# Optimization experiments

Measured on AMD Instinct MI355X. Metric: run time of the kernel, lower is better.

## Reference

```python
import jax, jax.numpy as jnp
import numpy as np

N_FFT = 512
HOP = 128
WIN = 512
LENGTH = 600  # hardcoded in the original forward


def _hann(n):
    # torch.hann_window default is periodic: 0.5*(1-cos(2*pi*i/n))
    i = jnp.arange(n, dtype=jnp.float32)
    return 0.5 * (1.0 - jnp.cos(2.0 * jnp.pi * i / n))


def setup_inputs() -> dict:
    key = jax.random.key(0)
    x = jax.random.normal(key, (8192, 1, 257, 6, 2), dtype=jnp.float32)
    return {"x": x}


def reference(x):
    B, C, F, T, D = x.shape  # C==1, F==n_fft//2+1, D==2
    # view(B, F, T, D) + view_as_complex
    spec = x[:, 0, :, :, 0] + 1j * x[:, 0, :, :, 1]          # [B, F, T] complex64
    # inverse real FFT per frame (torch.istft, normalized=False, onesided=True)
    frames = jnp.fft.irfft(spec.transpose(0, 2, 1), n=N_FFT, axis=-1)  # [B, T, n_fft]
    win = _hann(WIN)                                          # [n_fft] (win_length == n_fft)
    frames = frames * win                                     # synthesis windowing
    # overlap-add
    L = HOP * (T - 1) + N_FFT
    idx = jnp.arange(T)[:, None] * HOP + jnp.arange(N_FFT)[None, :]  # [T, n_fft]
    y = jnp.zeros((B, L), dtype=frames.dtype).at[:, idx].add(frames)  # [B, L]
    # window-square envelope normalization (COLA division)
    env = jnp.zeros((L,), dtype=frames.dtype).at[idx].add(win * win)  # [L]
    # center=True trim of n_fft//2, then length=600 crop
    start = N_FFT // 2
    sig = y[:, start:start + LENGTH] / env[start:start + LENGTH]       # [B, 600]
    return sig[:, None, :]                                    # unsqueeze(1) -> [B, 1, 600]
```

## Files before the change

### kernel.cpp

```cpp
#include <hip/hip_runtime.h>
#include <hip/hip_bf16.h>


#define NFFT   512
#define HOP    128
#define KDIM   3084
#define KP     3136
#define NOUT   600
#define NP     640
#define BM     64
#define BN     128
#define BK     64
#define KSTEPS (KP / BK)
#define LDA    72

#define NFRAG_K 98
#define FRAG_SH 512
#define WTOT    ((size_t)(NP / 16) * NFRAG_K * FRAG_SH)
#define NKSPLIT 4
#define GRIDB   (128 * 5 * NKSPLIT)

typedef short s16x8 __attribute__((ext_vector_type(8)));
typedef float f32x4 __attribute__((ext_vector_type(4)));

static __device__ __forceinline__ unsigned short bf16_bits(float f) {
    __hip_bfloat16 b = __float2bfloat16(f);
    return *(unsigned short*)&b;
}

static __device__ __forceinline__ void lds_barrier() {
    asm volatile("s_waitcnt lgkmcnt(0)" ::: "memory");
    __builtin_amdgcn_s_barrier();
    asm volatile("" ::: "memory");
}

__global__ __launch_bounds__(256) void gen_W(unsigned short* __restrict__ Wt,
                                             float4* __restrict__ outZ,
                                             int nvec4) {
    __shared__ float costab[512];
    __shared__ __align__(16) unsigned short rowbuf[KP];
    const int l   = blockIdx.x;
    const int tid = threadIdx.x;
    const float w0 = 6.283185307179586f / 512.0f;

    for (int i = blockIdx.x * 256 + tid; i < nvec4; i += NP * 256)
        outZ[i] = make_float4(0.f, 0.f, 0.f, 0.f);

    *(int4*)(rowbuf + tid * 8) = make_int4(0, 0, 0, 0);
    if (tid < 136) *(int4*)(rowbuf + (256 + tid) * 8) = make_int4(0, 0, 0, 0);
    costab[tid]       = __cosf((float)tid * w0);
    costab[tid + 256] = __cosf((float)(tid + 256) * w0);
    __syncthreads();

    if (l < NOUT) {
        const int p = l + 256;
        float env = 0.0f;
#pragma unroll
        for (int tt = 0; tt < 6; ++tt) {
            int m = p - HOP * tt;
            if (m >= 0 && m < NFFT) {
                float w = 0.5f - 0.5f * costab[m];
                env += w * w;
            }
        }
        const float inv = 1.0f / (512.0f * env);
        for (int f = tid; f <= 256; f += 256) {
            float cf = (f == 0 || f == 256) ? 1.0f : 2.0f;
#pragma unroll
            for (int t = 0; t < 6; ++t) {
                int n = p - HOP * t;
                if (n >= 0 && n < NFFT) {
                    float w = 0.5f - 0.5f * costab[n];
                    float scale = cf * w * inv;
                    int a = (f * n) & 511;
                    float c = costab[a];
                    float s = costab[(a + 384) & 511];
                    rowbuf[f * 12 + t * 2 + 0] = bf16_bits(scale * c);
                    rowbuf[f * 12 + t * 2 + 1] = bf16_bits(-scale * s);
                }
            }
        }
    }
    __syncthreads();

    const int n16 = l >> 4, r = l & 15;
    for (int u = tid; u < 392; u += 256) {
        const int kc = u >> 2, q = u & 3;
        int4 val = *(const int4*)(rowbuf + kc * 32 + q * 8);
        *(int4*)(Wt + (((size_t)n16 * NFRAG_K + kc) * 64 + q * 16 + r) * 8) = val;
    }
}

__global__ __launch_bounds__(256, 4) void gemm_kernel(
        const float* __restrict__ X,
        const unsigned short* __restrict__ Wt,
        float* __restrict__ out) {
    __shared__ __align__(16) unsigned short As[2 * BM * LDA];

    const int tid = threadIdx.x;
    const int bid  = blockIdx.x;
    const int xcd  = bid & 7;
    const int rest = bid >> 3;
    const int mt   = xcd * 16 + rest / 20;
    const int sub  = rest % 20;
    const int nt   = sub >> 2;
    const int kidx = sub & 3;
    const int mBase = mt * BM;
    const int nBase = nt * BN;
    const int sBeg  = (kidx * KSTEPS) / NKSPLIT;
    const int sEnd  = ((kidx + 1) * KSTEPS) / NKSPLIT;

    const int lane = tid & 63;
    const int wave = tid >> 6;
    const int wm   = (wave & 1) * 32;
    const int wn   = (wave >> 1) * 64;
    const int lrow = lane & 15;
    const int quad = lane >> 4;

    const int aRow = tid >> 4, aU = tid & 15;
    const float* aPtr = X + (size_t)(mBase + aRow) * KDIM + sBeg * BK + aU * 4;
    const int aColBase = aU * 4;
    const size_t aRowStride = (size_t)16 * KDIM;

    const int n16base = nt * 8 + (wave >> 1) * 4;
    const unsigned short* wB0 = Wt + (size_t)n16base * NFRAG_K * FRAG_SH
                                   + (size_t)lane * 8;

    f32x4 acc[2][4];
#pragma unroll
    for (int i = 0; i < 2; ++i)
#pragma unroll
        for (int j = 0; j < 4; ++j) acc[i][j] = (f32x4){0.f, 0.f, 0.f, 0.f};

#define ISSUE_A(AV, s)                                                         \
    {                                                                          \
        const int k0_ = (s) * BK;                                              \
        _Pragma("unroll")                                                      \
        for (int p = 0; p < 4; ++p) {                                          \
            AV[p] = make_float4(0.f, 0.f, 0.f, 0.f);                           \
            if (k0_ + aColBase < KDIM)                                         \
                AV[p] = *(const float4*)(aPtr + (size_t)((s) - sBeg) * BK +    \
                                         p * aRowStride);                      \
        }                                                                      \
    }

#define ISSUE_B4(BV, s, ks)                                                    \
    {                                                                          \
        const size_t kc_ = (size_t)(2 * (s) + (ks));                           \
        _Pragma("unroll")                                                      \
        for (int j = 0; j < 4; ++j)                                            \
            BV[j] = *(const s16x8*)(const void*)(wB0 +                         \
                        ((size_t)j * NFRAG_K + kc_) * FRAG_SH);                \
    }

#define STAGE_A(AV, ABASE)                                                     \
    {                                                                          \
        _Pragma("unroll")                                                      \
        for (int p = 0; p < 4; ++p) {                                          \
            float4 v = AV[p];                                                  \
            unsigned long long pk = (unsigned long long)bf16_bits(v.x) |       \
                                    ((unsigned long long)bf16_bits(v.y) << 16) |\
                                    ((unsigned long long)bf16_bits(v.z) << 32) |\
                                    ((unsigned long long)bf16_bits(v.w) << 48); \
            *(unsigned long long*)(As + (ABASE) + (aRow + 16 * p) * LDA +      \
                                   aU * 4) = pk;                               \
        }                                                                      \
    }

#define COMPUTE_KS(ks, ABASE, BV)                                              \
    {                                                                          \
        const int koff = (ks) * 32 + quad * 8;                                 \
        s16x8 afr0 = *(const s16x8*)(const void*)(As + (ABASE) +               \
                         (wm + lrow) * LDA + koff);                            \
        s16x8 afr1 = *(const s16x8*)(const void*)(As + (ABASE) +               \
                         (wm + 16 + lrow) * LDA + koff);                       \
        _Pragma("unroll")                                                      \
        for (int j = 0; j < 4; ++j)                                            \
            acc[0][j] = __builtin_amdgcn_mfma_f32_16x16x32_bf16(               \
                afr0, BV[j], acc[0][j], 0, 0, 0);                              \
        _Pragma("unroll")                                                      \
        for (int j = 0; j < 4; ++j)                                            \
            acc[1][j] = __builtin_amdgcn_mfma_f32_16x16x32_bf16(               \
                afr1, BV[j], acc[1][j], 0, 0, 0);                              \
    }

    float4 avH[4];
    s16x8  bv0[4], bv1[4];
    ISSUE_A(avH, sBeg);
    ISSUE_B4(bv0, sBeg, 0);
    ISSUE_B4(bv1, sBeg, 1);
    STAGE_A(avH, 0);
    ISSUE_A(avH, sBeg + 1);
    lds_barrier();

    int ard = 0;
    for (int step = sBeg; step < sEnd; ++step) {
        const int awr = ard ^ (BM * LDA);
        if (step + 1 < sEnd) {
            STAGE_A(avH, awr);
            if (step + 2 < sEnd) ISSUE_A(avH, step + 2);
        }
        COMPUTE_KS(0, ard, bv0);
        if (step + 1 < sEnd) ISSUE_B4(bv0, step + 1, 0);
        COMPUTE_KS(1, ard, bv1);
        if (step + 1 < sEnd) ISSUE_B4(bv1, step + 1, 1);
        lds_barrier();
        ard = awr;
    }

#undef ISSUE_A
#undef ISSUE_B4
#undef STAGE_A
#undef COMPUTE_KS

#pragma unroll
    for (int i = 0; i < 2; ++i) {
#pragma unroll
        for (int j = 0; j < 4; ++j) {
            int gn = nBase + wn + j * 16 + lrow;
            if (gn < NOUT) {
#pragma unroll
                for (int r = 0; r < 4; ++r) {
                    int gm = mBase + wm + i * 16 + quad * 4 + r;
                    atomicAdd(out + (size_t)gm * NOUT + gn, acc[i][j][r]);
                }
            }
        }
    }
}

extern "C" void kernel_launch(void* const* d_in, const int* in_sizes, int n_in,
                              void* d_out, int out_size, void* d_ws, size_t ws_size,
                              hipStream_t stream) {
    const float* X = (const float*)d_in[0];
    unsigned short* W = (unsigned short*)d_ws;
    float* out = (float*)d_out;

    gen_W<<<dim3(NP), 256, 0, stream>>>(W, (float4*)d_out, out_size / 4);
    gemm_kernel<<<dim3(GRIDB), 256, 0, stream>>>(X, W, out);
}
```

Baseline: 265.0 us.

## Double M tile to 128 and peel the K tail into a direct-load epilogue

Raises the GEMM block tile from 64 to 128 rows, so each wave computes a 64x64 sub-tile and every loaded B fragment feeds twice as many MFMAs. This halves the grid and lowers the occupancy hint to 3. The K loop now runs 12 full steps per split with no bounds checks. The leftover 32-wide K fragment is handled by the last split, which reads A straight from global memory with per-element guards. The goal is better B reuse and fewer A-load branches, at the cost of more registers, fewer blocks and a scalar tail path.

Result: faster. 259.5 us (-2.1%).

```diff
diff --git a/kernel.cpp b/kernel.cpp
--- a/kernel.cpp
+++ b/kernel.cpp
@@ -8,17 +8,17 @@
 #define KP     3136
 #define NOUT   600
 #define NP     640
-#define BM     64
+#define BM     128
 #define BN     128
 #define BK     64
-#define KSTEPS (KP / BK)
 #define LDA    72
+#define ABUF   (BM * LDA)
 
 #define NFRAG_K 98
 #define FRAG_SH 512
 #define WTOT    ((size_t)(NP / 16) * NFRAG_K * FRAG_SH)
 #define NKSPLIT 4
-#define GRIDB   (128 * 5 * NKSPLIT)
+#define GRIDB   (64 * 5 * NKSPLIT)
 
 typedef short s16x8 __attribute__((ext_vector_type(8)));
 typedef float f32x4 __attribute__((ext_vector_type(4)));
@@ -91,121 +91,131 @@
     }
 }
 
-__global__ __launch_bounds__(256, 4) void gemm_kernel(
+__global__ __launch_bounds__(256, 3) void gemm_kernel(
         const float* __restrict__ X,
         const unsigned short* __restrict__ Wt,
         float* __restrict__ out) {
-    __shared__ __align__(16) unsigned short As[2 * BM * LDA];
+    __shared__ __align__(16) unsigned short As[2 * ABUF];
 
     const int tid = threadIdx.x;
     const int bid  = blockIdx.x;
     const int xcd  = bid & 7;
     const int rest = bid >> 3;
-    const int mt   = xcd * 16 + rest / 20;
+    const int mt   = xcd * 8 + rest / 20;
     const int sub  = rest % 20;
     const int nt   = sub >> 2;
     const int kidx = sub & 3;
     const int mBase = mt * BM;
     const int nBase = nt * BN;
-    const int sBeg  = (kidx * KSTEPS) / NKSPLIT;
-    const int sEnd  = ((kidx + 1) * KSTEPS) / NKSPLIT;
+    const int sBeg  = kidx * 12;
+    const int sEnd  = sBeg + 12;
 
     const int lane = tid & 63;
     const int wave = tid >> 6;
-    const int wm   = (wave & 1) * 32;
-    const int wn   = (wave >> 1) * 64;
+    const int wm2  = (wave & 1) * 64;
+    const int wn2  = (wave >> 1) * 64;
     const int lrow = lane & 15;
     const int quad = lane >> 4;
 
-    const int aRow = tid >> 4, aU = tid & 15;
-    const float* aPtr = X + (size_t)(mBase + aRow) * KDIM + sBeg * BK + aU * 4;
-    const int aColBase = aU * 4;
+    const int aRowS = tid >> 4, aU = tid & 15;
+    const float* aPtr = X + (size_t)(mBase + aRowS) * KDIM + sBeg * BK + aU * 4;
     const size_t aRowStride = (size_t)16 * KDIM;
 
     const int n16base = nt * 8 + (wave >> 1) * 4;
     const unsigned short* wB0 = Wt + (size_t)n16base * NFRAG_K * FRAG_SH
                                    + (size_t)lane * 8;
 
-    f32x4 acc[2][4];
-#pragma unroll
-    for (int i = 0; i < 2; ++i)
+    f32x4 acc[4][4];
+#pragma unroll
+    for (int i = 0; i < 4; ++i)
 #pragma unroll
         for (int j = 0; j < 4; ++j) acc[i][j] = (f32x4){0.f, 0.f, 0.f, 0.f};
 
-#define ISSUE_A(AV, s)                                                         \
-    {                                                                          \
-        const int k0_ = (s) * BK;                                              \
-        _Pragma("unroll")                                                      \
-        for (int p = 0; p < 4; ++p) {                                          \
-            AV[p] = make_float4(0.f, 0.f, 0.f, 0.f);                           \
-            if (k0_ + aColBase < KDIM)                                         \
-                AV[p] = *(const float4*)(aPtr + (size_t)((s) - sBeg) * BK +    \
-                                         p * aRowStride);                      \
-        }                                                                      \
-    }
-
-#define ISSUE_B4(BV, s, ks)                                                    \
-    {                                                                          \
-        const size_t kc_ = (size_t)(2 * (s) + (ks));                           \
+#define ISSUE_A(s)                                                             \
+    {                                                                          \
+        const float* b_ = aPtr + (size_t)((s) - sBeg) * BK;                    \
+        _Pragma("unroll")                                                      \
+        for (int p = 0; p < 8; ++p)                                            \
+            avH[p] = *(const float4*)(b_ + (size_t)p * aRowStride);            \
+    }
+
+#define ISSUE_B4(BV, kc_)                                                      \
+    {                                                                          \
         _Pragma("unroll")                                                      \
         for (int j = 0; j < 4; ++j)                                            \
             BV[j] = *(const s16x8*)(const void*)(wB0 +                         \
-                        ((size_t)j * NFRAG_K + kc_) * FRAG_SH);                \
-    }
-
-#define STAGE_A(AV, ABASE)                                                     \
-    {                                                                          \
-        _Pragma("unroll")                                                      \
-        for (int p = 0; p < 4; ++p) {                                          \
-            float4 v = AV[p];                                                  \
+                        ((size_t)j * NFRAG_K + (size_t)(kc_)) * FRAG_SH);      \
+    }
+
+#define STAGE_A(AB)                                                            \
+    {                                                                          \
+        _Pragma("unroll")                                                      \
+        for (int p = 0; p < 8; ++p) {                                          \
+            float4 v = avH[p];                                                 \
             unsigned long long pk = (unsigned long long)bf16_bits(v.x) |       \
                                     ((unsigned long long)bf16_bits(v.y) << 16) |\
                                     ((unsigned long long)bf16_bits(v.z) << 32) |\
                                     ((unsigned long long)bf16_bits(v.w) << 48); \
-            *(unsigned long long*)(As + (ABASE) + (aRow + 16 * p) * LDA +      \
+            *(unsigned long long*)(As + (AB) + (aRowS + 16 * p) * LDA +        \
                                    aU * 4) = pk;                               \
         }                                                                      \
     }
 
-#define COMPUTE_KS(ks, ABASE, BV)                                              \
+#define COMPUTE_KS(AB, ks, BV)                                                 \
     {                                                                          \
         const int koff = (ks) * 32 + quad * 8;                                 \
-        s16x8 afr0 = *(const s16x8*)(const void*)(As + (ABASE) +               \
-                         (wm + lrow) * LDA + koff);                            \
-        s16x8 afr1 = *(const s16x8*)(const void*)(As + (ABASE) +               \
-                         (wm + 16 + lrow) * LDA + koff);                       \
-        _Pragma("unroll")                                                      \
-        for (int j = 0; j < 4; ++j)                                            \
-            acc[0][j] = __builtin_amdgcn_mfma_f32_16x16x32_bf16(               \
-                afr0, BV[j], acc[0][j], 0, 0, 0);                              \
-        _Pragma("unroll")                                                      \
-        for (int j = 0; j < 4; ++j)                                            \
-            acc[1][j] = __builtin_amdgcn_mfma_f32_16x16x32_bf16(               \
-                afr1, BV[j], acc[1][j], 0, 0, 0);                              \
-    }
-
-    float4 avH[4];
+        _Pragma("unroll")                                                      \
+        for (int i = 0; i < 4; ++i) {                                          \
+            s16x8 afr = *(const s16x8*)(const void*)(As + (AB) +               \
+                            (wm2 + i * 16 + lrow) * LDA + koff);               \
+            _Pragma("unroll")                                                  \
+            for (int j = 0; j < 4; ++j)                                        \
+                acc[i][j] = __builtin_amdgcn_mfma_f32_16x16x32_bf16(           \
+                    afr, BV[j], acc[i][j], 0, 0, 0);                           \
+        }                                                                      \
+    }
+
+    float4 avH[8];
     s16x8  bv0[4], bv1[4];
-    ISSUE_A(avH, sBeg);
-    ISSUE_B4(bv0, sBeg, 0);
-    ISSUE_B4(bv1, sBeg, 1);
-    STAGE_A(avH, 0);
-    ISSUE_A(avH, sBeg + 1);
+    ISSUE_A(sBeg);
+    ISSUE_B4(bv0, 2 * sBeg);
+    ISSUE_B4(bv1, 2 * sBeg + 1);
+    STAGE_A(0);
+    ISSUE_A(sBeg + 1);
     lds_barrier();
 
     int ard = 0;
     for (int step = sBeg; step < sEnd; ++step) {
-        const int awr = ard ^ (BM * LDA);
+        const int awr = ard ^ ABUF;
         if (step + 1 < sEnd) {
-            STAGE_A(avH, awr);
-            if (step + 2 < sEnd) ISSUE_A(avH, step + 2);
-        }
-        COMPUTE_KS(0, ard, bv0);
-        if (step + 1 < sEnd) ISSUE_B4(bv0, step + 1, 0);
-        COMPUTE_KS(1, ard, bv1);
-        if (step + 1 < sEnd) ISSUE_B4(bv1, step + 1, 1);
+            STAGE_A(awr);
+            if (step + 2 < sEnd) ISSUE_A(step + 2);
+        }
+        COMPUTE_KS(ard, 0, bv0);
+        if (step + 1 < sEnd) ISSUE_B4(bv0, 2 * (step + 1));
+        COMPUTE_KS(ard, 1, bv1);
+        if (step + 1 < sEnd) ISSUE_B4(bv1, 2 * (step + 1) + 1);
         lds_barrier();
         ard = awr;
+    }
+
+    if (kidx == 3) {
+        const int kb = 96 * 32 + quad * 8;
+        ISSUE_B4(bv0, 96);
+#pragma unroll
+        for (int i = 0; i < 4; ++i) {
+            const float* aR = X + (size_t)(mBase + wm2 + i * 16 + lrow) * KDIM;
+            s16x8 af;
+#pragma unroll
+            for (int e = 0; e < 8; ++e) {
+                const int k = kb + e;
+                af[e] = (short)bf16_bits(k < KDIM ? aR[k] : 0.f);
+            }
+#pragma unroll
+            for (int j = 0; j < 4; ++j)
+                acc[i][j] = __builtin_amdgcn_mfma_f32_16x16x32_bf16(
+                    af, bv0[j], acc[i][j], 0, 0, 0);
+        }
     }
 
 #undef ISSUE_A
@@ -214,14 +224,14 @@
 #undef COMPUTE_KS
 
 #pragma unroll
-    for (int i = 0; i < 2; ++i) {
+    for (int i = 0; i < 4; ++i) {
 #pragma unroll
         for (int j = 0; j < 4; ++j) {
-            int gn = nBase + wn + j * 16 + lrow;
+            int gn = nBase + wn2 + j * 16 + lrow;
             if (gn < NOUT) {
 #pragma unroll
                 for (int r = 0; r < 4; ++r) {
-                    int gm = mBase + wm + i * 16 + quad * 4 + r;
+                    int gm = mBase + wm2 + i * 16 + quad * 4 + r;
                     atomicAdd(out + (size_t)gm * NOUT + gn, acc[i][j][r]);
                 }
             }
```
